# Optimization experiments

Hardware: AMD Instinct MI355X
Metric: run time of the kernel (lower is better)

Reference implementation:

```python
import jax, jax.numpy as jnp
import numpy as np
from jax import lax

N, D, K, R, T = 200000, 128, 64, 4, 50000
L = 2 * R  # positive + negative relation layers
ITERATIONS = 2


def _l2norm(x, eps=1e-12):
    # torch F.normalize(p=2): x / max(||x||, eps)
    n = jnp.sqrt(jnp.sum(x * x, axis=-1, keepdims=True))
    return x / jnp.maximum(n, eps)


def setup_inputs() -> dict:
    key = jax.random.key(0)
    ks = jax.random.split(key, 8)
    # Unique write targets (a permutation) so the last-write scatter is deterministic;
    # matches input_specs' randint intent (indices uniform in [0, N)).
    perm = jax.random.permutation(ks[0], N)
    subj_idx = perm[:T].astype(jnp.int32)
    obj_idx = perm[T:2 * T].astype(jnp.int32)
    layer_idx = jax.random.randint(ks[1], (T,), 0, L, dtype=jnp.int32)
    memberships = jax.random.randint(ks[2], (N, K), 0, 2, dtype=jnp.int32)
    embedding_m = jax.random.normal(ks[3], (N, D), dtype=jnp.float32)
    # ClassUpdate params: [d+K] -> d
    Wc = jax.random.normal(ks[4], (D + K, D), dtype=jnp.float32) / np.sqrt(D + K)
    bc = jnp.zeros((D,), dtype=jnp.float32)
    # RelationUpdate params, one layer per (relation, polarity): [2d] -> [2d]
    Wr = jax.random.normal(ks[5], (L, 2 * D, 2 * D), dtype=jnp.float32) / np.sqrt(2 * D)
    br = jnp.zeros((L, 2 * D), dtype=jnp.float32)
    return {
        'embedding_m': embedding_m,
        'memberships': memberships,
        'subj_idx': subj_idx,
        'obj_idx': obj_idx,
        'layer_idx': layer_idx,
        'Wc': Wc, 'bc': bc, 'Wr': Wr, 'br': br,
    }


def reference(embedding_m, memberships, subj_idx, obj_idx, layer_idx, Wc, bc, Wr, br):
    mem = memberships.astype(embedding_m.dtype)  # [N, K]
    t_ar = jnp.arange(T)

    def iteration(e, _):
        # --- ClassUpdate: e' = l2norm(tanh([e; m] Wc + bc)) ---
        x = jnp.concatenate([e, mem], axis=1)           # [N, d+K]
        e = _l2norm(jnp.tanh(x @ Wc + bc))              # [N, d]
        # --- RelationUpdates: reads come from the post-class-update snapshot `e`
        pair = jnp.concatenate([e[subj_idx], e[obj_idx]], axis=1)   # [T, 2d]
        # compute through all L relation layers, then select each triple's layer
        out_all = jnp.einsum('tc,lcd->tld', pair, Wr) + br          # [T, L, 2d]
        out = jnp.tanh(out_all[t_ar, layer_idx])                    # [T, 2d]
        new_s = _l2norm(out[:, :D])
        new_o = _l2norm(out[:, D:])
        e_next = e.at[subj_idx].set(new_s).at[obj_idx].set(new_o)
        return e_next, None

    e_final, _ = lax.scan(iteration, embedding_m, None, length=ITERATIONS)
    return e_final
```

## Files before the change

### kernel.cpp

```cpp
#include <hip/hip_runtime.h>
#include <hip/hip_bf16.h>


#define NROWS 200000
#define DD    128
#define KK    64
#define TT    50000
#define LL    8
#define BT    64
#define PADT  50560

#define NB    100
#define CHB   500
#define PL    8
#define PREPB 268

#define WS_OFFS   0
#define WS_CNT    64
#define WS_BASE   4096
#define WS_BINS   8192
#define WS_WCP    210432
#define WS_WRP    (WS_WCP + 6*8*64*16)
#define WS_MB     (WS_WRP + 8*8*16*64*16)
#define WS_E16    (WS_MB + NROWS*8)
#define WS_NEED   (WS_E16 + (size_t)NROWS*DD*2)

typedef unsigned short u16;
typedef unsigned int   u32;
typedef unsigned long long u64;
typedef unsigned char  u8;
typedef __attribute__((ext_vector_type(8))) short bf16x8;
typedef __attribute__((ext_vector_type(4))) float f32x4;

#define SWZ(row, byte) ((byte) ^ (((row)&7)<<4))

__device__ __forceinline__ u32 bfbits(float f){
  __hip_bfloat16 h = __float2bfloat16(f);
  return (u32)*reinterpret_cast<unsigned short*>(&h);
}
__device__ __forceinline__ u32 pk(float lo, float hi){
  return bfbits(lo) | (bfbits(hi) << 16);
}
__device__ __forceinline__ float qreduce16(float ss){
  ss += __shfl_xor(ss, 1, 64);
  ss += __shfl_xor(ss, 2, 64);
  ss += __shfl_xor(ss, 4, 64);
  ss += __shfl_xor(ss, 8, 64);
  return ss;
}
__device__ __forceinline__ float fast_tanh(float x){
  float a = fabsf(x);
  float e = __expf(-2.0f*a);
  float t = (1.0f - e) * __builtin_amdgcn_rcpf(1.0f + e);
  return copysignf(t, x);
}
__device__ __forceinline__ float rnorm_scale(float ss){
  return __builtin_amdgcn_rcpf(fmaxf(__builtin_amdgcn_sqrtf(ss), 1e-12f));
}

__global__ __launch_bounds__(256) void k_prep(
    const float* __restrict__ Wc, const float* __restrict__ Wr,
    uint4* __restrict__ wcp, uint4* __restrict__ wrp,
    const int* __restrict__ layer, int* __restrict__ cnt)
{
  if (blockIdx.x >= PREPB){
    const int bb = blockIdx.x - PREPB, lane = threadIdx.x;
    if (lane >= 64) return;
    const int lim = bb*CHB + CHB;
    int i0 = bb*CHB + lane*PL, i1 = i0 + PL; if (i1 > lim) i1 = lim;
    int c[LL] = {0,0,0,0,0,0,0,0};
    for (int i = i0; i < i1; ++i){
      int l = layer[i];
      #pragma unroll
      for (int k = 0; k < LL; ++k) c[k] += (l == k);
    }
    #pragma unroll
    for (int k = 0; k < LL; ++k){
      int v = c[k];
      v += __shfl_xor(v, 1, 64); v += __shfl_xor(v, 2, 64);
      v += __shfl_xor(v, 4, 64); v += __shfl_xor(v, 8, 64);
      v += __shfl_xor(v, 16, 64); v += __shfl_xor(v, 32, 64);
      if (lane == k) cnt[bb*LL + k] = v;
    }
    return;
  }
  int id = blockIdx.x*blockDim.x + threadIdx.x;
  if (id < 3072){
    int lane = id & 63, nt = (id >> 6) & 7, kt = id >> 9;
    int k0 = kt*32 + (lane>>4)*8, n = nt*16 + (lane&15);
    u32 p[4];
    #pragma unroll
    for (int e2 = 0; e2 < 4; ++e2)
      p[e2] = pk(Wc[(k0 + 2*e2)*DD + n], Wc[(k0 + 2*e2 + 1)*DD + n]);
    wcp[id] = make_uint4(p[0], p[1], p[2], p[3]);
  } else if (id < 3072 + 65536){
    int id2 = id - 3072;
    int lane = id2 & 63, nt = (id2>>6) & 15, kt = (id2>>10) & 7, l = id2 >> 13;
    int k0 = kt*32 + (lane>>4)*8, n = nt*16 + (lane&15);
    const float* w = Wr + (size_t)l*65536;
    u32 p[4];
    #pragma unroll
    for (int e2 = 0; e2 < 4; ++e2)
      p[e2] = pk(w[(k0 + 2*e2)*256 + n], w[(k0 + 2*e2 + 1)*256 + n]);
    wrp[id2] = make_uint4(p[0], p[1], p[2], p[3]);
  }
}

__global__ __launch_bounds__(64) void k_bin2(const int* __restrict__ cnt,
                                             int* __restrict__ offs,
                                             int* __restrict__ gbase,
                                             int* __restrict__ bins)
{
  __shared__ int pre[NB][LL];
  __shared__ int tot[LL], soffs[LL+1];
  const int t = threadIdx.x;
  if (t < LL){
    int acc = 0;
    for (int bb = 0; bb < NB; ++bb){ pre[bb][t] = acc; acc += cnt[bb*LL + t]; }
    tot[t] = acc;
  }
  __syncthreads();
  if (t == 0){
    int acc = 0;
    for (int l = 0; l < LL; ++l){
      soffs[l] = acc; offs[l] = acc;
      acc += ((tot[l] + BT - 1)/BT)*BT;
    }
    soffs[LL] = acc; offs[LL] = acc;
  }
  __syncthreads();
  for (int idx = t; idx < NB*LL; idx += 64){
    int bb = idx >> 3, k = idx & 7;
    gbase[idx] = soffs[k] + pre[bb][k];
  }
  const int k = t >> 3, sub = t & 7;
  const int sz = soffs[k+1] - soffs[k];
  for (int i = tot[k] + sub; i < sz; i += 8) bins[soffs[k] + i] = -1;
}

__global__ __launch_bounds__(64) void k_bin3(const int* __restrict__ layer,
                                             const int* __restrict__ gbase,
                                             int* __restrict__ bins)
{
  const int bb = blockIdx.x, lane = threadIdx.x;
  const int lim = bb*CHB + CHB;
  int i0 = bb*CHB + lane*PL, i1 = i0 + PL; if (i1 > lim) i1 = lim;
  int c[LL] = {0,0,0,0,0,0,0,0};
  for (int i = i0; i < i1; ++i){
    int l = layer[i];
    #pragma unroll
    for (int k = 0; k < LL; ++k) c[k] += (l == k);
  }
  int start[LL];
  #pragma unroll
  for (int k = 0; k < LL; ++k){
    int v = c[k];
    #pragma unroll
    for (int d = 1; d < 64; d <<= 1){
      int u = __shfl_up(v, d, 64);
      if (lane >= d) v += u;
    }
    start[k] = gbase[bb*LL + k] + v - c[k];
  }
  for (int i = i0; i < i1; ++i){
    int l = layer[i];
    #pragma unroll
    for (int k = 0; k < LL; ++k)
      if (l == k) bins[start[k]++] = i;
  }
}

template<bool S16, bool MBITS, bool W16, bool WF32>
__global__ __launch_bounds__(256) void k_class(
    const float* __restrict__ srcf, const u16* __restrict__ src16,
    u16* __restrict__ e16, float* __restrict__ dstf,
    const int* __restrict__ mem, u64* __restrict__ mbits,
    const uint4* __restrict__ wcp, const float* __restrict__ bc)
{
  __shared__ u16   sA[64*192];
  __shared__ float sBc[DD];
  __shared__ float sPart[64][4];

  const int tid = threadIdx.x;
  const int lane = tid & 63, wid = tid >> 6;
  const int colj = lane & 15, qw = lane >> 4;

  bf16x8 wf[6][2];
  #pragma unroll
  for (int kt = 0; kt < 6; ++kt)
    #pragma unroll
    for (int j = 0; j < 2; ++j)
      wf[kt][j] = *(const bf16x8*)&wcp[(kt*8 + 2*wid + j)*64 + lane];
  if (tid < DD) sBc[tid] = bc[tid];

  const float b0 = bc[(2*wid)*16 + colj];
  const float b1 = bc[(2*wid+1)*16 + colj];
  (void)sBc;

  for (int rb = blockIdx.x; rb < NROWS/64; rb += gridDim.x){
    const int rowbase = rb * 64;
    __syncthreads();
    #pragma unroll
    for (int v = 0; v < 4; ++v){
      int f = (v*256 + tid) * 8;
      int row = f >> 7, col = f & 127;
      uint4 out;
      if constexpr (S16){
        out = *(const uint4*)(src16 + (size_t)(rowbase+row)*DD + col);
      } else {
        const float4* s4 = (const float4*)(srcf + (size_t)(rowbase+row)*DD + col);
        float4 a = s4[0], b = s4[1];
        out = make_uint4(pk(a.x,a.y), pk(a.z,a.w), pk(b.x,b.y), pk(b.z,b.w));
      }
      *(uint4*)((char*)sA + row*384 + SWZ(row, col*2)) = out;
    }
    if constexpr (MBITS){
      const int r = tid >> 2, q = tid & 3;
      u64 m = mbits[rowbase + r];
      u32 s = (u32)(m >> (q*16)) & 0xFFFFu;
      u32 p[8];
      #pragma unroll
      for (int jj = 0; jj < 8; ++jj){
        u32 lo = (s >> (2*jj))     & 1u;
        u32 hi = (s >> (2*jj + 1)) & 1u;
        p[jj] = (lo ? 0x3F80u : 0u) | (hi ? 0x3F800000u : 0u);
      }
      *(uint4*)((char*)sA + r*384 + SWZ(r, 256 + q*32))      = make_uint4(p[0],p[1],p[2],p[3]);
      *(uint4*)((char*)sA + r*384 + SWZ(r, 256 + q*32 + 16)) = make_uint4(p[4],p[5],p[6],p[7]);
    } else {
      u8* mb8 = (u8*)mbits;
      #pragma unroll
      for (int v = 0; v < 2; ++v){
        int f = (v*256 + tid) * 8;
        int row = f >> 6, col = f & 63;
        const int4* s4 = (const int4*)(mem + (size_t)(rowbase+row)*KK + col);
        int4 a = s4[0], b = s4[1];
        u32 p0 = (a.x?0x3F80u:0u) | ((a.y?0x3F80u:0u)<<16);
        u32 p1 = (a.z?0x3F80u:0u) | ((a.w?0x3F80u:0u)<<16);
        u32 p2 = (b.x?0x3F80u:0u) | ((b.y?0x3F80u:0u)<<16);
        u32 p3 = (b.z?0x3F80u:0u) | ((b.w?0x3F80u:0u)<<16);
        *(uint4*)((char*)sA + row*384 + SWZ(row, 256 + col*2)) =
          make_uint4(p0, p1, p2, p3);
        u8 byte = (u8)((a.x!=0) | ((a.y!=0)<<1) | ((a.z!=0)<<2) | ((a.w!=0)<<3)
                 | ((b.x!=0)<<4) | ((b.y!=0)<<5) | ((b.z!=0)<<6) | ((b.w!=0)<<7));
        mb8[(size_t)(rowbase+row)*8 + (col>>3)] = byte;
      }
    }
    __syncthreads();

    f32x4 acc[4][2];
    #pragma unroll
    for (int m = 0; m < 4; ++m){
      acc[m][0] = (f32x4){0.f,0.f,0.f,0.f};
      acc[m][1] = (f32x4){0.f,0.f,0.f,0.f};
    }
    #pragma unroll
    for (int m = 0; m < 4; ++m){
      int row = m*16 + colj;
      #pragma unroll
      for (int kt = 0; kt < 6; ++kt){
        bf16x8 afr = *(bf16x8*)((char*)sA + row*384 + SWZ(row, kt*64 + qw*16));
        acc[m][0] = __builtin_amdgcn_mfma_f32_16x16x32_bf16(afr, wf[kt][0], acc[m][0], 0,0,0);
        acc[m][1] = __builtin_amdgcn_mfma_f32_16x16x32_bf16(afr, wf[kt][1], acc[m][1], 0,0,0);
      }
    }
    #pragma unroll
    for (int m = 0; m < 4; ++m){
      #pragma unroll
      for (int r = 0; r < 4; ++r){
        float t0 = fast_tanh(acc[m][0][r] + b0);
        float t1 = fast_tanh(acc[m][1][r] + b1);
        acc[m][0][r] = t0; acc[m][1][r] = t1;
        float ss = qreduce16(t0*t0 + t1*t1);
        if (colj == 0) sPart[m*16 + qw*4 + r][wid] = ss;
      }
    }
    __syncthreads();
    #pragma unroll
    for (int m = 0; m < 4; ++m){
      #pragma unroll
      for (int r = 0; r < 4; ++r){
        int tri = m*16 + qw*4 + r;
        f32x4 p = *(f32x4*)sPart[tri];
        float sc = rnorm_scale(p[0] + p[1] + p[2] + p[3]);
        int grow = rowbase + tri;
        float v0 = acc[m][0][r]*sc, v1 = acc[m][1][r]*sc;
        int c0 = (2*wid)*16 + colj;
        if constexpr (W16){
          e16[(size_t)grow*DD + c0]      = (u16)bfbits(v0);
          e16[(size_t)grow*DD + c0 + 16] = (u16)bfbits(v1);
        }
        if constexpr (WF32){
          dstf[(size_t)grow*DD + c0]      = v0;
          dstf[(size_t)grow*DD + c0 + 16] = v1;
        }
      }
    }
  }
}

template<bool S16, bool W16, bool WF32>
__global__ __launch_bounds__(256) void k_rel(
    const float* __restrict__ ef32, u16* __restrict__ e16,
    float* __restrict__ dstf,
    const int* __restrict__ subj, const int* __restrict__ obj,
    const uint4* __restrict__ wrp, const float* __restrict__ br,
    const int* __restrict__ offs, const int* __restrict__ bins)
{
  __shared__ u16   sA[64*256];
  __shared__ float sBr[256];
  __shared__ float sPart[BT][4];
  __shared__ int   sS[BT], sO[BT];

  const int tid  = threadIdx.x;
  const int base = blockIdx.x * BT;
  if (base >= offs[LL]) return;
  int l = 0;
  while (l < LL-1 && base >= offs[l+1]) ++l;

  const int lane = tid & 63, wid = tid >> 6;
  const int colj = lane & 15, qw = lane >> 4;

  const uint4* wb = wrp + (size_t)l*8192 + lane;
  bf16x8 wf[8][4];
  #pragma unroll
  for (int n = 0; n < 4; ++n){
    wf[0][n] = *(const bf16x8*)&wb[(0*16 + wid*4 + n)*64];
    wf[1][n] = *(const bf16x8*)&wb[(1*16 + wid*4 + n)*64];
  }

  sBr[tid] = br[l*256 + tid];

  const int ti = tid >> 2, q = tid & 3;
  int id = bins[base + ti];
  int rs = -1, ro = -1;
  if (id >= 0){ rs = subj[id]; ro = obj[id]; }
  if (q == 0){ sS[ti] = rs; sO[ti] = ro; }
  const int rr = (q < 2) ? rs : ro;
  if constexpr (S16){
    const u16* srcp = e16 + (size_t)rr*DD + (q & 1)*64;
    #pragma unroll
    for (int j = 0; j < 8; ++j){
      uint4 w = (id >= 0) ? ((const uint4*)srcp)[j] : make_uint4(0u,0u,0u,0u);
      *(uint4*)((char*)sA + ti*512 + SWZ(ti, q*128 + j*16)) = w;
    }
  } else {
    const float* srcp = ef32 + (size_t)rr*DD + (q & 1)*64;
    #pragma unroll
    for (int j = 0; j < 8; ++j){
      uint4 w;
      if (id >= 0){
        float4 a = ((const float4*)srcp)[2*j], b = ((const float4*)srcp)[2*j+1];
        w = make_uint4(pk(a.x,a.y), pk(a.z,a.w), pk(b.x,b.y), pk(b.z,b.w));
      } else w = make_uint4(0u,0u,0u,0u);
      *(uint4*)((char*)sA + ti*512 + SWZ(ti, q*128 + j*16)) = w;
    }
  }
  __syncthreads();

  f32x4 acc[4][4];
  #pragma unroll
  for (int m = 0; m < 4; ++m)
    #pragma unroll
    for (int n = 0; n < 4; ++n) acc[m][n] = (f32x4){0.f,0.f,0.f,0.f};

  #pragma unroll
  for (int kt = 0; kt < 8; ++kt){
    if (kt + 2 < 8){
      #pragma unroll
      for (int n = 0; n < 4; ++n)
        wf[kt+2][n] = *(const bf16x8*)&wb[((kt+2)*16 + wid*4 + n)*64];
    }
    #pragma unroll
    for (int m = 0; m < 4; ++m){
      int row = m*16 + colj;
      bf16x8 afr = *(bf16x8*)((char*)sA + row*512 + SWZ(row, kt*64 + qw*16));
      #pragma unroll
      for (int n = 0; n < 4; ++n)
        acc[m][n] = __builtin_amdgcn_mfma_f32_16x16x32_bf16(afr, wf[kt][n], acc[m][n], 0,0,0);
    }
  }

  #pragma unroll
  for (int m = 0; m < 4; ++m){
    #pragma unroll
    for (int n = 0; n < 4; ++n){
      float b = sBr[(wid*4 + n)*16 + colj];
      #pragma unroll
      for (int r = 0; r < 4; ++r)
        acc[m][n][r] = fast_tanh(acc[m][n][r] + b);
    }
    #pragma unroll
    for (int r = 0; r < 4; ++r){
      float ss = acc[m][0][r]*acc[m][0][r] + acc[m][1][r]*acc[m][1][r]
               + acc[m][2][r]*acc[m][2][r] + acc[m][3][r]*acc[m][3][r];
      ss = qreduce16(ss);
      if (colj == 0) sPart[m*16 + qw*4 + r][wid] = ss;
    }
  }
  __syncthreads();

  const int h = wid >> 1;
  #pragma unroll
  for (int m = 0; m < 4; ++m){
    #pragma unroll
    for (int r = 0; r < 4; ++r){
      int tri = m*16 + qw*4 + r;
      int row = h ? sO[tri] : sS[tri];
      if (row < 0) continue;
      float ss = sPart[tri][2*h] + sPart[tri][2*h + 1];
      float sc = rnorm_scale(ss);
      #pragma unroll
      for (int n = 0; n < 4; ++n){
        int cc = (wid*4 + n)*16 + colj - h*DD;
        float v = acc[m][n][r]*sc;
        if constexpr (W16)
          e16[(size_t)row*DD + cc] = (u16)bfbits(v);
        if constexpr (WF32)
          dstf[(size_t)row*DD + cc] = v;
      }
    }
  }
}

extern "C" void kernel_launch(void* const* d_in, const int* in_sizes, int n_in,
                              void* d_out, int out_size, void* d_ws, size_t ws_size,
                              hipStream_t stream) {
  (void)in_sizes; (void)n_in; (void)out_size;
  const float* emb  = (const float*)d_in[0];
  const int*   mem  = (const int*)  d_in[1];
  const int*   subj = (const int*)  d_in[2];
  const int*   obj  = (const int*)  d_in[3];
  const int*   lay  = (const int*)  d_in[4];
  const float* Wc   = (const float*)d_in[5];
  const float* bc   = (const float*)d_in[6];
  const float* Wr   = (const float*)d_in[7];
  const float* br   = (const float*)d_in[8];

  float* e   = (float*)d_out;
  char*  wsb = (char*)d_ws;
  int*   offs  = (int*)(wsb + WS_OFFS);
  int*   cnt   = (int*)(wsb + WS_CNT);
  int*   gbase = (int*)(wsb + WS_BASE);
  int*   bins  = (int*)(wsb + WS_BINS);
  uint4* wcp   = (uint4*)(wsb + WS_WCP);
  uint4* wrp   = (uint4*)(wsb + WS_WRP);
  u64*   mbits = (u64*)(wsb + WS_MB);
  u16*   e16   = (u16*)(wsb + WS_E16);

  k_prep<<<PREPB + NB, 256, 0, stream>>>(Wc, Wr, wcp, wrp, lay, cnt);
  k_bin2<<<1, 64, 0, stream>>>(cnt, offs, gbase, bins);
  k_bin3<<<NB, 64, 0, stream>>>(lay, gbase, bins);

  if (ws_size >= WS_NEED){
    k_class<false,false,true,false><<<1024, 256, 0, stream>>>(
        emb, nullptr, e16, nullptr, mem, mbits, wcp, bc);
    k_rel<true,true,false><<<PADT/BT, 256, 0, stream>>>(
        nullptr, e16, nullptr, subj, obj, wrp, br, offs, bins);
    k_class<true,true,false,true><<<1024, 256, 0, stream>>>(
        nullptr, e16, nullptr, e, mem, mbits, wcp, bc);
    k_rel<false,false,true><<<PADT/BT, 256, 0, stream>>>(
        e, nullptr, e, subj, obj, wrp, br, offs, bins);
  } else {
    k_class<false,false,false,true><<<1024, 256, 0, stream>>>(
        emb, nullptr, nullptr, e, mem, mbits, wcp, bc);
    k_rel<false,false,true><<<PADT/BT, 256, 0, stream>>>(
        e, nullptr, e, subj, obj, wrp, br, offs, bins);
    k_class<false,true,false,true><<<1024, 256, 0, stream>>>(
        e, nullptr, nullptr, e, mem, mbits, wcp, bc);
    k_rel<false,false,true><<<PADT/BT, 256, 0, stream>>>(
        e, nullptr, e, subj, obj, wrp, br, offs, bins);
  }
}
```

Measured before the change: 184.2 us.

## Prefetch next row tile into registers and pack memberships in prep kernel

The membership bit-packing moves out of the first class-update pass into extra blocks of the prep kernel, so both class passes read packed bits instead of the int32 membership matrix. The class kernel now loads the next 64-row tile of embeddings and membership bits into registers while the MFMA work for the current tile runs, hiding global load latency. The shared-memory tile is split into separate embedding and membership arrays with an XOR swizzle. The cost is higher register pressure from holding a prefetched tile per thread, plus extra prep blocks that read the full membership matrix.

```diff
diff --git a/kernel.cpp b/kernel.cpp
--- a/kernel.cpp
+++ b/kernel.cpp
@@ -9,11 +9,14 @@
 #define LL    8
 #define BT    64
 #define PADT  50560
+#define NPASS 3125
+#define GRIDC 1024
 
 #define NB    100
 #define CHB   500
 #define PL    8
 #define PREPB 268
+#define MBB   6250
 
 #define WS_OFFS   0
 #define WS_CNT    64
@@ -61,8 +64,17 @@
 __global__ __launch_bounds__(256) void k_prep(
     const float* __restrict__ Wc, const float* __restrict__ Wr,
     uint4* __restrict__ wcp, uint4* __restrict__ wrp,
-    const int* __restrict__ layer, int* __restrict__ cnt)
+    const int* __restrict__ layer, int* __restrict__ cnt,
+    const int* __restrict__ mem, u8* __restrict__ mb8)
 {
+  if (blockIdx.x >= PREPB + NB){
+    int gid = (blockIdx.x - PREPB - NB)*256 + threadIdx.x;
+    const int4* s4 = (const int4*)(mem + (size_t)gid*8);
+    int4 a = s4[0], b = s4[1];
+    mb8[gid] = (u8)((a.x!=0) | ((a.y!=0)<<1) | ((a.z!=0)<<2) | ((a.w!=0)<<3)
+             | ((b.x!=0)<<4) | ((b.y!=0)<<5) | ((b.z!=0)<<6) | ((b.w!=0)<<7));
+    return;
+  }
   if (blockIdx.x >= PREPB){
     const int bb = blockIdx.x - PREPB, lane = threadIdx.x;
     if (lane >= 64) return;
@@ -170,20 +182,21 @@
   }
 }
 
-template<bool S16, bool MBITS, bool W16, bool WF32>
+template<bool S16, bool W16, bool WF32>
 __global__ __launch_bounds__(256) void k_class(
     const float* __restrict__ srcf, const u16* __restrict__ src16,
     u16* __restrict__ e16, float* __restrict__ dstf,
-    const int* __restrict__ mem, u64* __restrict__ mbits,
+    const u64* __restrict__ mbits,
     const uint4* __restrict__ wcp, const float* __restrict__ bc)
 {
-  __shared__ u16   sA[64*192];
-  __shared__ float sBc[DD];
+  __shared__ __align__(16) u16 sE[64*128];
+  __shared__ __align__(16) u16 sM[64*64];
   __shared__ float sPart[64][4];
 
   const int tid = threadIdx.x;
   const int lane = tid & 63, wid = tid >> 6;
   const int colj = lane & 15, qw = lane >> 4;
+  const int r7 = colj & 7;
 
   bf16x8 wf[6][2];
   #pragma unroll
@@ -191,33 +204,45 @@
     #pragma unroll
     for (int j = 0; j < 2; ++j)
       wf[kt][j] = *(const bf16x8*)&wcp[(kt*8 + 2*wid + j)*64 + lane];
-  if (tid < DD) sBc[tid] = bc[tid];
-
   const float b0 = bc[(2*wid)*16 + colj];
   const float b1 = bc[(2*wid+1)*16 + colj];
-  (void)sBc;
-
-  for (int rb = blockIdx.x; rb < NROWS/64; rb += gridDim.x){
-    const int rowbase = rb * 64;
-    __syncthreads();
-    #pragma unroll
-    for (int v = 0; v < 4; ++v){
-      int f = (v*256 + tid) * 8;
-      int row = f >> 7, col = f & 127;
+
+  const int erow = tid >> 2, ec = tid & 3;
+  const int mrow = tid >> 2, mq = tid & 3;
+
+  int rb = blockIdx.x;
+  uint4  E16[4];
+  float4 EF[8];
+  u64    mv;
+  {
+    const size_t rowoff = (size_t)(rb*64 + erow)*DD + ec*32;
+    if constexpr (S16){
+      const uint4* gp = (const uint4*)(src16 + rowoff);
+      #pragma unroll
+      for (int k = 0; k < 4; ++k) E16[k] = gp[k];
+    } else {
+      const float4* gp = (const float4*)(srcf + rowoff);
+      #pragma unroll
+      for (int k = 0; k < 8; ++k) EF[k] = gp[k];
+    }
+    mv = mbits[rb*64 + mrow];
+  }
+
+  for (;;){
+    #pragma unroll
+    for (int k = 0; k < 4; ++k){
+      int chunk = ec*4 + k;
       uint4 out;
       if constexpr (S16){
-        out = *(const uint4*)(src16 + (size_t)(rowbase+row)*DD + col);
+        out = E16[k];
       } else {
-        const float4* s4 = (const float4*)(srcf + (size_t)(rowbase+row)*DD + col);
-        float4 a = s4[0], b = s4[1];
+        float4 a = EF[2*k], b = EF[2*k+1];
         out = make_uint4(pk(a.x,a.y), pk(a.z,a.w), pk(b.x,b.y), pk(b.z,b.w));
       }
-      *(uint4*)((char*)sA + row*384 + SWZ(row, col*2)) = out;
-    }
-    if constexpr (MBITS){
-      const int r = tid >> 2, q = tid & 3;
-      u64 m = mbits[rowbase + r];
-      u32 s = (u32)(m >> (q*16)) & 0xFFFFu;
+      *(uint4*)((char*)sE + erow*256 + ((chunk ^ (erow&7)))*16) = out;
+    }
+    {
+      u32 s = (u32)(mv >> (mq*16)) & 0xFFFFu;
       u32 p[8];
       #pragma unroll
       for (int jj = 0; jj < 8; ++jj){
@@ -225,28 +250,28 @@
         u32 hi = (s >> (2*jj + 1)) & 1u;
         p[jj] = (lo ? 0x3F80u : 0u) | (hi ? 0x3F800000u : 0u);
       }
-      *(uint4*)((char*)sA + r*384 + SWZ(r, 256 + q*32))      = make_uint4(p[0],p[1],p[2],p[3]);
-      *(uint4*)((char*)sA + r*384 + SWZ(r, 256 + q*32 + 16)) = make_uint4(p[4],p[5],p[6],p[7]);
-    } else {
-      u8* mb8 = (u8*)mbits;
-      #pragma unroll
-      for (int v = 0; v < 2; ++v){
-        int f = (v*256 + tid) * 8;
-        int row = f >> 6, col = f & 63;
-        const int4* s4 = (const int4*)(mem + (size_t)(rowbase+row)*KK + col);
-        int4 a = s4[0], b = s4[1];
-        u32 p0 = (a.x?0x3F80u:0u) | ((a.y?0x3F80u:0u)<<16);
-        u32 p1 = (a.z?0x3F80u:0u) | ((a.w?0x3F80u:0u)<<16);
-        u32 p2 = (b.x?0x3F80u:0u) | ((b.y?0x3F80u:0u)<<16);
-        u32 p3 = (b.z?0x3F80u:0u) | ((b.w?0x3F80u:0u)<<16);
-        *(uint4*)((char*)sA + row*384 + SWZ(row, 256 + col*2)) =
-          make_uint4(p0, p1, p2, p3);
-        u8 byte = (u8)((a.x!=0) | ((a.y!=0)<<1) | ((a.z!=0)<<2) | ((a.w!=0)<<3)
-                 | ((b.x!=0)<<4) | ((b.y!=0)<<5) | ((b.z!=0)<<6) | ((b.w!=0)<<7));
-        mb8[(size_t)(rowbase+row)*8 + (col>>3)] = byte;
-      }
+      *(uint4*)((char*)sM + mrow*128 + (((2*mq  ) ^ (mrow&7)))*16) =
+          make_uint4(p[0],p[1],p[2],p[3]);
+      *(uint4*)((char*)sM + mrow*128 + (((2*mq+1) ^ (mrow&7)))*16) =
+          make_uint4(p[4],p[5],p[6],p[7]);
     }
     __syncthreads();
+
+    const int rbn = rb + GRIDC;
+    const bool more = (rbn < NPASS);
+    if (more){
+      const size_t rowoff = (size_t)(rbn*64 + erow)*DD + ec*32;
+      if constexpr (S16){
+        const uint4* gp = (const uint4*)(src16 + rowoff);
+        #pragma unroll
+        for (int k = 0; k < 4; ++k) E16[k] = gp[k];
+      } else {
+        const float4* gp = (const float4*)(srcf + rowoff);
+        #pragma unroll
+        for (int k = 0; k < 8; ++k) EF[k] = gp[k];
+      }
+      mv = mbits[rbn*64 + mrow];
+    }
 
     f32x4 acc[4][2];
     #pragma unroll
@@ -256,10 +281,16 @@
     }
     #pragma unroll
     for (int m = 0; m < 4; ++m){
-      int row = m*16 + colj;
-      #pragma unroll
-      for (int kt = 0; kt < 6; ++kt){
-        bf16x8 afr = *(bf16x8*)((char*)sA + row*384 + SWZ(row, kt*64 + qw*16));
+      const int row = m*16 + colj;
+      #pragma unroll
+      for (int kt = 0; kt < 4; ++kt){
+        bf16x8 afr = *(bf16x8*)((char*)sE + row*256 + (((kt*4+qw) ^ r7))*16);
+        acc[m][0] = __builtin_amdgcn_mfma_f32_16x16x32_bf16(afr, wf[kt][0], acc[m][0], 0,0,0);
+        acc[m][1] = __builtin_amdgcn_mfma_f32_16x16x32_bf16(afr, wf[kt][1], acc[m][1], 0,0,0);
+      }
+      #pragma unroll
+      for (int kt = 4; kt < 6; ++kt){
+        bf16x8 afr = *(bf16x8*)((char*)sM + row*128 + ((((kt-4)*4+qw) ^ r7))*16);
         acc[m][0] = __builtin_amdgcn_mfma_f32_16x16x32_bf16(afr, wf[kt][0], acc[m][0], 0,0,0);
         acc[m][1] = __builtin_amdgcn_mfma_f32_16x16x32_bf16(afr, wf[kt][1], acc[m][1], 0,0,0);
       }
@@ -276,6 +307,7 @@
       }
     }
     __syncthreads();
+    const int rowbase = rb*64;
     #pragma unroll
     for (int m = 0; m < 4; ++m){
       #pragma unroll
@@ -296,6 +328,8 @@
         }
       }
     }
+    if (!more) break;
+    rb = rbn;
   }
 }
 
@@ -446,28 +480,29 @@
   uint4* wcp   = (uint4*)(wsb + WS_WCP);
   uint4* wrp   = (uint4*)(wsb + WS_WRP);
   u64*   mbits = (u64*)(wsb + WS_MB);
+  u8*    mb8   = (u8*)(wsb + WS_MB);
   u16*   e16   = (u16*)(wsb + WS_E16);
 
-  k_prep<<<PREPB + NB, 256, 0, stream>>>(Wc, Wr, wcp, wrp, lay, cnt);
+  k_prep<<<PREPB + NB + MBB, 256, 0, stream>>>(Wc, Wr, wcp, wrp, lay, cnt, mem, mb8);
   k_bin2<<<1, 64, 0, stream>>>(cnt, offs, gbase, bins);
   k_bin3<<<NB, 64, 0, stream>>>(lay, gbase, bins);
 
   if (ws_size >= WS_NEED){
-    k_class<false,false,true,false><<<1024, 256, 0, stream>>>(
-        emb, nullptr, e16, nullptr, mem, mbits, wcp, bc);
+    k_class<false,true,false><<<GRIDC, 256, 0, stream>>>(
+        emb, nullptr, e16, nullptr, mbits, wcp, bc);
     k_rel<true,true,false><<<PADT/BT, 256, 0, stream>>>(
         nullptr, e16, nullptr, subj, obj, wrp, br, offs, bins);
-    k_class<true,true,false,true><<<1024, 256, 0, stream>>>(
-        nullptr, e16, nullptr, e, mem, mbits, wcp, bc);
+    k_class<true,false,true><<<GRIDC, 256, 0, stream>>>(
+        nullptr, e16, nullptr, e, mbits, wcp, bc);
     k_rel<false,false,true><<<PADT/BT, 256, 0, stream>>>(
         e, nullptr, e, subj, obj, wrp, br, offs, bins);
   } else {
-    k_class<false,false,false,true><<<1024, 256, 0, stream>>>(
-        emb, nullptr, nullptr, e, mem, mbits, wcp, bc);
+    k_class<false,false,true><<<GRIDC, 256, 0, stream>>>(
+        emb, nullptr, nullptr, e, mbits, wcp, bc);
     k_rel<false,false,true><<<PADT/BT, 256, 0, stream>>>(
         e, nullptr, e, subj, obj, wrp, br, offs, bins);
-    k_class<false,true,false,true><<<1024, 256, 0, stream>>>(
-        e, nullptr, nullptr, e, mem, mbits, wcp, bc);
+    k_class<false,false,true><<<GRIDC, 256, 0, stream>>>(
+        e, nullptr, nullptr, e, mbits, wcp, bc);
     k_rel<false,false,true><<<PADT/BT, 256, 0, stream>>>(
         e, nullptr, e, subj, obj, wrp, br, offs, bins);
   }
```

After: 196.2 us. +6.5%, slower.
